# Kernel optimization log

Hardware: AMD Instinct MI355X
Metric: run time of the kernel (lower is better)

The kernel has to match this reference:

```python
import jax, jax.numpy as jnp
import numpy as np

B, S, D, H = 64, 128, 1024, 8
DK = D // H  # 128 == S, required by the module's (attn@V)@V quirk
DFF = 2048
EPS = 1e-12


def layernorm(x, w, b):
    u = x.mean(-1, keepdims=True)
    s = ((x - u) ** 2).mean(-1, keepdims=True)
    return w * (x - u) / jnp.sqrt(s + EPS) + b


def setup_inputs() -> dict:
    key = jax.random.key(0)
    ks = jax.random.split(key, 10)
    w = lambda k, shape: jax.random.normal(k, shape, jnp.float32) * 0.02
    return {
        "x": jax.random.normal(ks[0], (B, S, D), jnp.float32),
        "mask": jnp.ones((1, 1, S, S), jnp.int32),
        "Wq": w(ks[1], (D, D)), "bq": jnp.zeros((D,), jnp.float32),
        "Wk": w(ks[2], (D, D)), "bk": jnp.zeros((D,), jnp.float32),
        "Wv": w(ks[3], (D, D)), "bv": jnp.zeros((D,), jnp.float32),
        "Wo": w(ks[4], (D, D)), "bo": jnp.zeros((D,), jnp.float32),
        "ln1_w": jnp.ones((D,), jnp.float32), "ln1_b": jnp.zeros((D,), jnp.float32),
        "W1": w(ks[5], (DFF, D)), "b1": jnp.zeros((DFF,), jnp.float32),
        "W2": w(ks[6], (4 * D, DFF)), "b2": jnp.zeros((4 * D,), jnp.float32),
        "W3": w(ks[7], (D, 4 * D)), "b3": jnp.zeros((D,), jnp.float32),
        "ln2_w": jnp.ones((D,), jnp.float32), "ln2_b": jnp.zeros((D,), jnp.float32),
    }


def reference(x, mask, Wq, bq, Wk, bk, Wv, bv, Wo, bo, ln1_w, ln1_b,
              W1, b1, W2, b2, W3, b3, ln2_w, ln2_b):
    # QKV projections -> [B, H, S, DK]
    Q = (x @ Wq.T + bq).reshape(B, S, H, DK).transpose(0, 2, 1, 3)
    K = (x @ Wk.T + bk).reshape(B, S, H, DK).transpose(0, 2, 1, 3)
    V = (x @ Wv.T + bv).reshape(B, S, H, DK).transpose(0, 2, 1, 3)

    scores = jnp.einsum('bhqd,bhkd->bhqk', Q, K) / jnp.sqrt(jnp.float32(DK))
    scores = jnp.where(mask == 0, jnp.float32(-1e9), scores)
    attn = jax.nn.softmax(scores, axis=-1)  # dropout = identity (eval)
    av = jnp.matmul(attn, V)                 # [B,H,S,DK]
    # Faithful quirk in the source: multiply by V a second time (DK == S).
    ctx = jnp.matmul(av, V)                  # [B,H,S,DK]
    ctx = ctx.transpose(0, 2, 1, 3).reshape(B, S, D)
    attn_out = ctx @ Wo.T + bo

    h = layernorm(x + attn_out, ln1_w, ln1_b)

    f = jax.nn.relu(h @ W1.T + b1)           # [B,S,DFF]
    f = jax.nn.relu(f @ W2.T + b2)           # [B,S,4D]
    f = f @ W3.T + b3                        # [B,S,D]

    return layernorm(h + f, ln2_w, ln2_b)
```

## Files before the change

### kernel.cpp

```cpp
#include <hip/hip_runtime.h>
#include <hip/hip_bf16.h>

using bf16 = __hip_bfloat16;
typedef __attribute__((ext_vector_type(4))) float f32x4;
typedef __attribute__((ext_vector_type(8))) short bf16x8;

__device__ __forceinline__ unsigned short bfbits(float f) {
    bf16 h = __float2bfloat16(f);
    return __builtin_bit_cast(unsigned short, h);
}

__device__ __forceinline__ void g2l16(const void* g, void* l) {
    __builtin_amdgcn_global_load_lds(
        (const __attribute__((address_space(1))) unsigned int*)g,
        (__attribute__((address_space(3))) unsigned int*)l, 16, 0, 0);
}

__global__ void castk(const float* __restrict__ in, bf16* __restrict__ out, int n4) {
    int stride = gridDim.x * blockDim.x;
    for (int i = blockIdx.x * blockDim.x + threadIdx.x; i < n4; i += stride) {
        float4 v = reinterpret_cast<const float4*>(in)[i];
        ushort4 o;
        o.x = bfbits(v.x); o.y = bfbits(v.y); o.z = bfbits(v.z); o.w = bfbits(v.w);
        reinterpret_cast<ushort4*>(out)[i] = o;
    }
}

template<int EPI, int SPLITK>
__global__ __launch_bounds__(512, 2)
void gemm256(const bf16* __restrict__ A, const bf16* __restrict__ Bm,
             int N, int ldk, int kloop,
             const float* __restrict__ bias0, const float* __restrict__ bias1,
             const float* __restrict__ bias2,
             void* __restrict__ outp,
             bf16* __restrict__ q_o, bf16* __restrict__ k_o, bf16* __restrict__ v_o) {
    __shared__ __align__(16) char lds[65536];
    const int tid = threadIdx.x;
    const int lane = tid & 63, wave = tid >> 6;
    const int rlo = lane & 15, g = lane >> 4;
    const int wr = wave >> 2, wc = wave & 3;
    const int nbn = N >> 8;
    const int nwg = gridDim.x;
    int wg = (int)blockIdx.x;
    wg = (wg & 7) * (nwg >> 3) + (wg >> 3);
    int slice = 0;
    if constexpr (SPLITK) {
        int half = nwg >> 1;
        slice = (wg >= half) ? 1 : 0;
        wg -= slice * half;
    }
    const int bm = wg / nbn, bn = wg % nbn;
    const size_t ldb = (size_t)ldk * 2;
    const char* abase = (const char*)A + ((size_t)bm << 8) * ldb + (size_t)slice * kloop * 2;
    const char* bbase = (const char*)Bm + ((size_t)bn << 8) * ldb + (size_t)slice * kloop * 2;

    const int P = tid * 16;
    const int R = P >> 7;
    const int qs = (P & 127) ^ ((R & 7) << 4);
    const size_t goff0 = (size_t)(R * 2 + (qs >> 6)) * ldb + (qs & 63);
    const size_t ghalf = (size_t)128 * ldb;

    const int o_in = (((rlo & 1) << 6) | (g << 4)) ^ (((rlo >> 1) & 7) << 4);
    const int aoff = wr * 8192 + (rlo >> 1) * 128 + o_in;
    const int boff = 16384 + (wc >> 1) * 8192 + (wc & 1) * 4096 + (rlo >> 1) * 128 + o_in;

    const f32x4 fz = {0.f, 0.f, 0.f, 0.f};
    f32x4 acc[8][4];
#pragma unroll
    for (int i = 0; i < 8; ++i)
#pragma unroll
        for (int j = 0; j < 4; ++j) acc[i][j] = fz;

    auto stA = [&](int buf, int h, int kt) {
        g2l16(abase + goff0 + (size_t)h * ghalf + (size_t)kt * 64,
              lds + buf * 32768 + h * 8192 + P);
    };
    auto stB = [&](int buf, int h, int kt) {
        g2l16(bbase + goff0 + (size_t)h * ghalf + (size_t)kt * 64,
              lds + buf * 32768 + 16384 + h * 8192 + P);
    };

    stA(0, 0, 0); stA(0, 1, 0); stB(0, 0, 0); stB(0, 1, 0);
    asm volatile("s_waitcnt vmcnt(0)" ::: "memory");
    __builtin_amdgcn_s_barrier();
    __builtin_amdgcn_sched_barrier(0);

    const int NT = kloop >> 5;
    for (int kt = 0; kt < NT; ++kt) {
        const char* lb = lds + (kt & 1) * 32768;
        const int nbuf = (kt & 1) ^ 1;
        const bool pre = (kt + 1) < NT;

        bf16x8 bfr[4], afr[8];
#pragma unroll
        for (int nf = 0; nf < 4; ++nf)
            bfr[nf] = *reinterpret_cast<const bf16x8*>(lb + nf * 1024 + boff);
#pragma unroll
        for (int i = 0; i < 8; ++i)
            afr[i] = *reinterpret_cast<const bf16x8*>(lb + i * 1024 + aoff);
        if (pre) { stA(nbuf, 0, kt + 1); stA(nbuf, 1, kt + 1);
                   stB(nbuf, 0, kt + 1); stB(nbuf, 1, kt + 1); }
        __builtin_amdgcn_s_setprio(1);
#pragma unroll
        for (int i = 0; i < 4; ++i)
#pragma unroll
            for (int nf = 0; nf < 4; ++nf)
                acc[i][nf] = __builtin_amdgcn_mfma_f32_16x16x32_bf16(afr[i], bfr[nf], acc[i][nf], 0, 0, 0);
#pragma unroll
        for (int i = 0; i < 4; ++i)
#pragma unroll
            for (int nf = 0; nf < 4; ++nf)
                acc[4 + i][nf] = __builtin_amdgcn_mfma_f32_16x16x32_bf16(afr[4 + i], bfr[nf], acc[4 + i][nf], 0, 0, 0);
        __builtin_amdgcn_s_setprio(0);

        if (pre) {
            asm volatile("s_waitcnt vmcnt(0)" ::: "memory");
            __builtin_amdgcn_s_barrier();
            __builtin_amdgcn_sched_barrier(0);
        }
    }

    const int gm0 = (bm << 8) + wr * 128;
    const int gn0 = (bn << 8) + wc * 64;
#pragma unroll
    for (int mf = 0; mf < 8; ++mf) {
#pragma unroll
        for (int nf = 0; nf < 4; ++nf) {
            const int gnc = gn0 + nf * 16 + rlo;
#pragma unroll
            for (int r = 0; r < 4; ++r) {
                const int gmr = gm0 + mf * 16 + g * 4 + r;
                float val = acc[mf][nf][r];
                if constexpr (EPI == 0) {
                    int t = gnc >> 10;
                    const float* bp = (t == 0) ? bias0 : ((t == 1) ? bias1 : bias2);
                    val += bp[gnc & 1023];
                    bf16* dst = (t == 0) ? q_o : ((t == 1) ? k_o : v_o);
                    int hh = (gnc >> 7) & 7, d = gnc & 127;
                    int bb = gmr >> 7, s = gmr & 127;
                    dst[(((size_t)bb * 8 + hh) * 128 + s) * 128 + d] = __float2bfloat16(val);
                } else if constexpr (EPI == 1) {
                    val = fmaxf(val + bias0[gnc], 0.f);
                    ((bf16*)outp)[(size_t)gmr * N + gnc] = __float2bfloat16(val);
                } else {
                    float* pp = (float*)outp + (size_t)slice * 8388608;
                    pp[(size_t)gmr * N + gnc] = val;
                }
            }
        }
    }
}

template<int EPI>
__global__ __launch_bounds__(256, 2)
void gemm_bt(const bf16* __restrict__ A, const bf16* __restrict__ Bm,
             int M, int N, int K,
             const float* __restrict__ bias0, const float* __restrict__ resid,
             void* __restrict__ outp) {
    (void)M;
    __shared__ __align__(16) char As[8192];
    __shared__ __align__(16) char Bs[8192];
    int tid = threadIdx.x, wave = tid >> 6, lane = tid & 63;
    int nbn = N >> 7;
    int bm = blockIdx.x / nbn, bn = blockIdx.x % nbn;
    int wm = (wave >> 1) << 6, wn = (wave & 1) << 6;
    int rlo = lane & 15, g = lane >> 4;

    const char* abase = (const char*)(A + (size_t)(bm << 7) * K);
    const char* bbase = (const char*)(Bm + (size_t)(bn << 7) * K);

    const f32x4 fzero = {0.f, 0.f, 0.f, 0.f};
    f32x4 acc[4][4];
#pragma unroll
    for (int i = 0; i < 4; ++i)
#pragma unroll
        for (int j = 0; j < 4; ++j) acc[i][j] = fzero;

    int L0 = wave * 2048 + lane * 16;
    size_t ldbyte = (size_t)K * 2;

    for (int k0 = 0; k0 < K; k0 += 32) {
#pragma unroll
        for (int j = 0; j < 2; ++j) {
            int L = L0 + j * 1024;
            int row = L >> 6;
            int cb = (L & 63) ^ (((row >> 1) & 3) << 4);
            g2l16(abase + (size_t)row * ldbyte + (size_t)k0 * 2 + cb, As + wave * 2048 + j * 1024);
            g2l16(bbase + (size_t)row * ldbyte + (size_t)k0 * 2 + cb, Bs + wave * 2048 + j * 1024);
        }
        __syncthreads();
        bf16x8 af[4], bf8[4];
#pragma unroll
        for (int i = 0; i < 4; ++i) {
            int ra = wm + i * 16 + rlo;
            af[i] = *reinterpret_cast<const bf16x8*>(As + ra * 64 + ((g * 16) ^ (((ra >> 1) & 3) << 4)));
            int rb = wn + i * 16 + rlo;
            bf8[i] = *reinterpret_cast<const bf16x8*>(Bs + rb * 64 + ((g * 16) ^ (((rb >> 1) & 3) << 4)));
        }
#pragma unroll
        for (int mi = 0; mi < 4; ++mi)
#pragma unroll
            for (int ni = 0; ni < 4; ++ni)
                acc[mi][ni] = __builtin_amdgcn_mfma_f32_16x16x32_bf16(af[mi], bf8[ni], acc[mi][ni], 0, 0, 0);
        __syncthreads();
    }

    int gm0 = (bm << 7) + wm, gn0 = (bn << 7) + wn;
#pragma unroll
    for (int mi = 0; mi < 4; ++mi) {
#pragma unroll
        for (int ni = 0; ni < 4; ++ni) {
            int gnc = gn0 + ni * 16 + rlo;
#pragma unroll
            for (int r = 0; r < 4; ++r) {
                int gmr = gm0 + mi * 16 + g * 4 + r;
                float val = acc[mi][ni][r];
                val += bias0[gnc] + resid[(size_t)gmr * N + gnc];
                ((float*)outp)[(size_t)gmr * N + gnc] = val;
            }
        }
    }
}

__global__ __launch_bounds__(256)
void transpose_v(const bf16* __restrict__ V, bf16* __restrict__ VT) {
    __shared__ unsigned short t[128 * 132];
    int bh = blockIdx.x, tid = threadIdx.x;
    const unsigned short* src = (const unsigned short*)(V + (size_t)bh * 16384);
#pragma unroll
    for (int i = 0; i < 8; ++i) {
        int idx = tid + i * 256;
        int srow = idx >> 4;
        int c8 = (idx & 15) * 8;
        ushort4 a = reinterpret_cast<const ushort4*>(src + srow * 128 + c8)[0];
        ushort4 b = reinterpret_cast<const ushort4*>(src + srow * 128 + c8 + 4)[0];
        reinterpret_cast<ushort4*>(t + srow * 132 + c8)[0] = a;
        reinterpret_cast<ushort4*>(t + srow * 132 + c8 + 4)[0] = b;
    }
    __syncthreads();
    unsigned short* dst = (unsigned short*)(VT + (size_t)bh * 16384);
#pragma unroll
    for (int i = 0; i < 8; ++i) {
        int idx = tid + i * 256;
        int drow = idx >> 4;
        int s8 = (idx & 15) * 8;
        ushort4 a, b;
        a.x = t[(s8 + 0) * 132 + drow]; a.y = t[(s8 + 1) * 132 + drow];
        a.z = t[(s8 + 2) * 132 + drow]; a.w = t[(s8 + 3) * 132 + drow];
        b.x = t[(s8 + 4) * 132 + drow]; b.y = t[(s8 + 5) * 132 + drow];
        b.z = t[(s8 + 6) * 132 + drow]; b.w = t[(s8 + 7) * 132 + drow];
        reinterpret_cast<ushort4*>(dst + drow * 128 + s8)[0] = a;
        reinterpret_cast<ushort4*>(dst + drow * 128 + s8 + 4)[0] = b;
    }
}

__global__ __launch_bounds__(256, 2)
void attn_scores(const bf16* __restrict__ Q, const bf16* __restrict__ K, bf16* __restrict__ P) {
    __shared__ __align__(16) char Qs[32768];
    __shared__ __align__(16) char Ks[32768];
    int bh = blockIdx.x;
    int tid = threadIdx.x, wave = tid >> 6, lane = tid & 63;
    const char* qsrc = (const char*)(Q + (size_t)bh * 16384);
    const char* ksrc = (const char*)(K + (size_t)bh * 16384);
#pragma unroll
    for (int j = 0; j < 8; ++j) {
        int L = wave * 8192 + j * 1024 + lane * 16;
        int row = L >> 8;
        int cb = (L & 255) ^ ((row & 7) << 4);
        g2l16(qsrc + row * 256 + cb, Qs + wave * 8192 + j * 1024);
        g2l16(ksrc + row * 256 + cb, Ks + wave * 8192 + j * 1024);
    }
    __syncthreads();
    int rlo = lane & 15, g = lane >> 4;
    const f32x4 fzero = {0.f, 0.f, 0.f, 0.f};
    f32x4 acc[2][8];
#pragma unroll
    for (int mi = 0; mi < 2; ++mi)
#pragma unroll
        for (int ni = 0; ni < 8; ++ni) acc[mi][ni] = fzero;
#pragma unroll
    for (int kk = 0; kk < 4; ++kk) {
        bf16x8 aq[2], bk8[8];
#pragma unroll
        for (int mi = 0; mi < 2; ++mi) {
            int row = wave * 32 + mi * 16 + rlo;
            aq[mi] = *reinterpret_cast<const bf16x8*>(Qs + row * 256 + ((kk * 64 + g * 16) ^ ((row & 7) << 4)));
        }
#pragma unroll
        for (int ni = 0; ni < 8; ++ni) {
            int row = ni * 16 + rlo;
            bk8[ni] = *reinterpret_cast<const bf16x8*>(Ks + row * 256 + ((kk * 64 + g * 16) ^ ((row & 7) << 4)));
        }
#pragma unroll
        for (int mi = 0; mi < 2; ++mi)
#pragma unroll
            for (int ni = 0; ni < 8; ++ni)
                acc[mi][ni] = __builtin_amdgcn_mfma_f32_16x16x32_bf16(aq[mi], bk8[ni], acc[mi][ni], 0, 0, 0);
    }
    const float scale = 0.088388347648318447f;
    unsigned short* pdst = (unsigned short*)(P + (size_t)bh * 16384);
#pragma unroll
    for (int mi = 0; mi < 2; ++mi) {
#pragma unroll
        for (int r = 0; r < 4; ++r) {
            float m = -3e38f;
#pragma unroll
            for (int ni = 0; ni < 8; ++ni) m = fmaxf(m, acc[mi][ni][r]);
#pragma unroll
            for (int o = 1; o < 16; o <<= 1) m = fmaxf(m, __shfl_xor(m, o));
            m *= scale;
            float e[8];
            float sum = 0.f;
#pragma unroll
            for (int ni = 0; ni < 8; ++ni) { e[ni] = __expf(acc[mi][ni][r] * scale - m); sum += e[ni]; }
#pragma unroll
            for (int o = 1; o < 16; o <<= 1) sum += __shfl_xor(sum, o);
            float inv = 1.f / sum;
            int qrow = wave * 32 + mi * 16 + g * 4 + r;
#pragma unroll
            for (int ni = 0; ni < 8; ++ni)
                pdst[qrow * 128 + ni * 16 + rlo] = bfbits(e[ni] * inv);
        }
    }
}

__global__ __launch_bounds__(256, 2)
void attn_ctx(const bf16* __restrict__ P, const bf16* __restrict__ VT, bf16* __restrict__ CTX) {
    __shared__ __align__(16) char Vs[32768];
    __shared__ __align__(16) char Ts[32768];
    int bh = blockIdx.x, b = bh >> 3, h = bh & 7;
    int tid = threadIdx.x, wave = tid >> 6, lane = tid & 63;
    const char* vsrc = (const char*)(VT + (size_t)bh * 16384);
#pragma unroll
    for (int j = 0; j < 8; ++j) {
        int L = wave * 8192 + j * 1024 + lane * 16;
        int row = L >> 8;
        int cb = (L & 255) ^ ((row & 7) << 4);
        g2l16(vsrc + row * 256 + cb, Vs + wave * 8192 + j * 1024);
    }
    __syncthreads();
    int rlo = lane & 15, g = lane >> 4;
    const char* psrc = (const char*)(P + (size_t)bh * 16384);
    const f32x4 fzero = {0.f, 0.f, 0.f, 0.f};
    f32x4 accT[2][8];
#pragma unroll
    for (int mi = 0; mi < 2; ++mi)
#pragma unroll
        for (int ni = 0; ni < 8; ++ni) accT[mi][ni] = fzero;
#pragma unroll
    for (int kk = 0; kk < 4; ++kk) {
        bf16x8 ap[2], bv8[8];
#pragma unroll
        for (int mi = 0; mi < 2; ++mi) {
            int row = wave * 32 + mi * 16 + rlo;
            ap[mi] = *reinterpret_cast<const bf16x8*>(psrc + (size_t)row * 256 + kk * 64 + g * 16);
        }
#pragma unroll
        for (int ni = 0; ni < 8; ++ni) {
            int row = ni * 16 + rlo;
            bv8[ni] = *reinterpret_cast<const bf16x8*>(Vs + row * 256 + ((kk * 64 + g * 16) ^ ((row & 7) << 4)));
        }
#pragma unroll
        for (int mi = 0; mi < 2; ++mi)
#pragma unroll
            for (int ni = 0; ni < 8; ++ni)
                accT[mi][ni] = __builtin_amdgcn_mfma_f32_16x16x32_bf16(ap[mi], bv8[ni], accT[mi][ni], 0, 0, 0);
    }
#pragma unroll
    for (int mi = 0; mi < 2; ++mi)
#pragma unroll
        for (int ni = 0; ni < 8; ++ni)
#pragma unroll
            for (int r = 0; r < 4; ++r) {
                int trow = wave * 32 + mi * 16 + g * 4 + r;
                int cbyte = ((ni * 16 + rlo) * 2) ^ ((trow & 7) << 4);
                *(unsigned short*)(Ts + trow * 256 + cbyte) = bfbits(accT[mi][ni][r]);
            }
    __syncthreads();
    f32x4 accC[2][8];
#pragma unroll
    for (int mi = 0; mi < 2; ++mi)
#pragma unroll
        for (int ni = 0; ni < 8; ++ni) accC[mi][ni] = fzero;
#pragma unroll
    for (int kk = 0; kk < 4; ++kk) {
        bf16x8 at[2], bv8[8];
#pragma unroll
        for (int mi = 0; mi < 2; ++mi) {
            int row = wave * 32 + mi * 16 + rlo;
            at[mi] = *reinterpret_cast<const bf16x8*>(Ts + row * 256 + ((kk * 64 + g * 16) ^ ((row & 7) << 4)));
        }
#pragma unroll
        for (int ni = 0; ni < 8; ++ni) {
            int row = ni * 16 + rlo;
            bv8[ni] = *reinterpret_cast<const bf16x8*>(Vs + row * 256 + ((kk * 64 + g * 16) ^ ((row & 7) << 4)));
        }
#pragma unroll
        for (int mi = 0; mi < 2; ++mi)
#pragma unroll
            for (int ni = 0; ni < 8; ++ni)
                accC[mi][ni] = __builtin_amdgcn_mfma_f32_16x16x32_bf16(at[mi], bv8[ni], accC[mi][ni], 0, 0, 0);
    }
    unsigned short* cdst = (unsigned short*)CTX;
#pragma unroll
    for (int mi = 0; mi < 2; ++mi)
#pragma unroll
        for (int ni = 0; ni < 8; ++ni)
#pragma unroll
            for (int r = 0; r < 4; ++r) {
                int q = wave * 32 + mi * 16 + g * 4 + r;
                int gm = b * 128 + q;
                int col = h * 128 + ni * 16 + rlo;
                cdst[(size_t)gm * 1024 + col] = bfbits(accC[mi][ni][r]);
            }
}

template<int MODE>
__global__ __launch_bounds__(256)
void ln_k(const float* __restrict__ Y, const float* __restrict__ w, const float* __restrict__ b,
          float* __restrict__ Hf, bf16* __restrict__ Hb) {
    int row = blockIdx.x, tid = threadIdx.x;
    float4 v = reinterpret_cast<const float4*>(Y + (size_t)row * 1024)[tid];
    float s = v.x + v.y + v.z + v.w;
    float q = v.x * v.x + v.y * v.y + v.z * v.z + v.w * v.w;
#pragma unroll
    for (int o = 1; o < 64; o <<= 1) { s += __shfl_xor(s, o); q += __shfl_xor(q, o); }
    __shared__ float ss[4], sq[4];
    if ((tid & 63) == 0) { ss[tid >> 6] = s; sq[tid >> 6] = q; }
    __syncthreads();
    s = ss[0] + ss[1] + ss[2] + ss[3];
    q = sq[0] + sq[1] + sq[2] + sq[3];
    float u = s * (1.f / 1024.f);
    float var = fmaxf(q * (1.f / 1024.f) - u * u, 0.f);
    float rstd = rsqrtf(var + 1e-12f);
    float4 wv = reinterpret_cast<const float4*>(w)[tid];
    float4 bv = reinterpret_cast<const float4*>(b)[tid];
    float o0 = wv.x * (v.x - u) * rstd + bv.x;
    float o1 = wv.y * (v.y - u) * rstd + bv.y;
    float o2 = wv.z * (v.z - u) * rstd + bv.z;
    float o3 = wv.w * (v.w - u) * rstd + bv.w;
    reinterpret_cast<float4*>(Hf + (size_t)row * 1024)[tid] = make_float4(o0, o1, o2, o3);
    if constexpr (MODE == 0) {
        ushort4 ob;
        ob.x = bfbits(o0); ob.y = bfbits(o1); ob.z = bfbits(o2); ob.w = bfbits(o3);
        reinterpret_cast<ushort4*>(Hb)[row * 256 + tid] = ob;
    }
}

__global__ __launch_bounds__(256)
void ln2k(const float* __restrict__ PA, const float* __restrict__ PB,
          const float* __restrict__ b3, const float* __restrict__ resid,
          const float* __restrict__ w, const float* __restrict__ b,
          float* __restrict__ out) {
    int row = blockIdx.x, tid = threadIdx.x;
    size_t off = (size_t)row * 256 + tid;
    float4 pa = reinterpret_cast<const float4*>(PA)[off];
    float4 pb = reinterpret_cast<const float4*>(PB)[off];
    float4 bi = reinterpret_cast<const float4*>(b3)[tid];
    float4 rs = reinterpret_cast<const float4*>(resid)[off];
    float4 v = make_float4(pa.x + pb.x + bi.x + rs.x, pa.y + pb.y + bi.y + rs.y,
                           pa.z + pb.z + bi.z + rs.z, pa.w + pb.w + bi.w + rs.w);
    float s = v.x + v.y + v.z + v.w;
    float q = v.x * v.x + v.y * v.y + v.z * v.z + v.w * v.w;
#pragma unroll
    for (int o = 1; o < 64; o <<= 1) { s += __shfl_xor(s, o); q += __shfl_xor(q, o); }
    __shared__ float ss[4], sq[4];
    if ((tid & 63) == 0) { ss[tid >> 6] = s; sq[tid >> 6] = q; }
    __syncthreads();
    s = ss[0] + ss[1] + ss[2] + ss[3];
    q = sq[0] + sq[1] + sq[2] + sq[3];
    float u = s * (1.f / 1024.f);
    float var = fmaxf(q * (1.f / 1024.f) - u * u, 0.f);
    float rstd = rsqrtf(var + 1e-12f);
    float4 wv = reinterpret_cast<const float4*>(w)[tid];
    float4 bv = reinterpret_cast<const float4*>(b)[tid];
    float4 o4;
    o4.x = wv.x * (v.x - u) * rstd + bv.x;
    o4.y = wv.y * (v.y - u) * rstd + bv.y;
    o4.z = wv.z * (v.z - u) * rstd + bv.z;
    o4.w = wv.w * (v.w - u) * rstd + bv.w;
    reinterpret_cast<float4*>(out)[off] = o4;
}

extern "C" void kernel_launch(void* const* d_in, const int* in_sizes, int n_in,
                              void* d_out, int out_size, void* d_ws, size_t ws_size,
                              hipStream_t stream) {
    (void)in_sizes; (void)n_in; (void)out_size; (void)ws_size;
    const float* x    = (const float*)d_in[0];
    const float* Wq   = (const float*)d_in[2];
    const float* bq   = (const float*)d_in[3];
    const float* Wk   = (const float*)d_in[4];
    const float* bk   = (const float*)d_in[5];
    const float* Wv   = (const float*)d_in[6];
    const float* bv   = (const float*)d_in[7];
    const float* Wo   = (const float*)d_in[8];
    const float* bo   = (const float*)d_in[9];
    const float* ln1w = (const float*)d_in[10];
    const float* ln1b = (const float*)d_in[11];
    const float* W1   = (const float*)d_in[12];
    const float* b1   = (const float*)d_in[13];
    const float* W2   = (const float*)d_in[14];
    const float* b2   = (const float*)d_in[15];
    const float* W3   = (const float*)d_in[16];
    const float* b3   = (const float*)d_in[17];
    const float* ln2w = (const float*)d_in[18];
    const float* ln2b = (const float*)d_in[19];

    char* ws = (char*)d_ws;
    bf16*  XB    = (bf16*)(ws + 0);
    bf16*  WQKVB = (bf16*)(ws + 16777216);
    bf16*  WOB   = (bf16*)(ws + 23068672);
    bf16*  W1B   = (bf16*)(ws + 25165824);
    bf16*  W2B   = (bf16*)(ws + 29360128);
    bf16*  W3B   = (bf16*)(ws + 46137344);
    bf16*  Qb    = (bf16*)(ws + 54525952);
    bf16*  Kb    = (bf16*)(ws + 71303168);
    bf16*  Vb    = (bf16*)(ws + 88080384);
    bf16*  VTb   = (bf16*)(ws + 104857600);
    bf16*  Pb    = (bf16*)(ws + 121634816);
    bf16*  CTX   = (bf16*)(ws + 138412032);
    float* Y2    = (float*)(ws + 155189248);
    float* H32   = (float*)(ws + 188743680);
    bf16*  HB    = (bf16*)(ws + 222298112);
    bf16*  F1    = (bf16*)(ws + 155189248);
    bf16*  F2    = (bf16*)(ws + 54525952);
    float* PW3   = (float*)(ws + 121634816);

    auto cast = [&](const float* s, bf16* dd, int n4) {
        int nb = (n4 + 255) / 256; if (nb > 2048) nb = 2048;
        castk<<<nb, 256, 0, stream>>>(s, dd, n4);
    };
    cast(x,  XB,             2097152);
    cast(Wq, WQKVB,           262144);
    cast(Wk, WQKVB + 1048576, 262144);
    cast(Wv, WQKVB + 2097152, 262144);
    cast(Wo, WOB,             262144);
    cast(W1, W1B,             524288);
    cast(W2, W2B,            2097152);
    cast(W3, W3B,            1048576);

    gemm256<0, 0><<<384, 512, 0, stream>>>(XB, WQKVB, 3072, 1024, 1024,
                                           bq, bk, bv, nullptr, Qb, Kb, Vb);
    transpose_v<<<512, 256, 0, stream>>>(Vb, VTb);
    attn_scores<<<512, 256, 0, stream>>>(Qb, Kb, Pb);
    attn_ctx<<<512, 256, 0, stream>>>(Pb, VTb, CTX);
    gemm_bt<2><<<512, 256, 0, stream>>>(CTX, WOB, 8192, 1024, 1024, bo, x, (void*)Y2);
    ln_k<0><<<8192, 256, 0, stream>>>(Y2, ln1w, ln1b, H32, HB);
    gemm256<1, 0><<<256, 512, 0, stream>>>(HB, W1B, 2048, 1024, 1024,
                                           b1, nullptr, nullptr, (void*)F1, nullptr, nullptr, nullptr);
    gemm256<1, 0><<<512, 512, 0, stream>>>(F1, W2B, 4096, 2048, 2048,
                                           b2, nullptr, nullptr, (void*)F2, nullptr, nullptr, nullptr);
    gemm256<2, 1><<<256, 512, 0, stream>>>(F2, W3B, 1024, 4096, 2048,
                                           nullptr, nullptr, nullptr, (void*)PW3, nullptr, nullptr, nullptr);
    ln2k<<<8192, 256, 0, stream>>>(PW3, PW3 + 8388608, b3, H32, ln2w, ln2b, (float*)d_out);
}
```

Measured before the change: 459.2 us.

## Deepen GEMM K-tile to 64 with 4-phase interleaved LDS staging pipeline

The 256x256 bf16 GEMM kernel now uses a 64-wide K tile with 128KB of LDS double buffering. Each iteration is split into four MFMA phases interleaved with partial LDS fragment loads and staggered global-to-LDS prefetches. A is prefetched two tiles ahead and B one tile ahead. The aim is to halve loop iterations and hide global and LDS latency behind MFMA work. In exchange it adds many more barriers, and 128KB of LDS likely drops occupancy from 2 workgroups per CU to 1.

```diff
diff --git a/kernel.cpp b/kernel.cpp
--- a/kernel.cpp
+++ b/kernel.cpp
@@ -34,7 +34,7 @@
              const float* __restrict__ bias2,
              void* __restrict__ outp,
              bf16* __restrict__ q_o, bf16* __restrict__ k_o, bf16* __restrict__ v_o) {
-    __shared__ __align__(16) char lds[65536];
+    __shared__ __align__(16) char lds[131072];
     const int tid = threadIdx.x;
     const int lane = tid & 63, wave = tid >> 6;
     const int rlo = lane & 15, g = lane >> 4;
@@ -54,15 +54,38 @@
     const char* abase = (const char*)A + ((size_t)bm << 8) * ldb + (size_t)slice * kloop * 2;
     const char* bbase = (const char*)Bm + ((size_t)bn << 8) * ldb + (size_t)slice * kloop * 2;
 
-    const int P = tid * 16;
-    const int R = P >> 7;
-    const int qs = (P & 127) ^ ((R & 7) << 4);
-    const size_t goff0 = (size_t)(R * 2 + (qs >> 6)) * ldb + (qs & 63);
-    const size_t ghalf = (size_t)128 * ldb;
-
-    const int o_in = (((rlo & 1) << 6) | (g << 4)) ^ (((rlo >> 1) & 7) << 4);
-    const int aoff = wr * 8192 + (rlo >> 1) * 128 + o_in;
-    const int boff = 16384 + (wc >> 1) * 8192 + (wc & 1) * 4096 + (rlo >> 1) * 128 + o_in;
+    auto stage = [&](int bufbyte, int region, int h, const char* gbase, int kt) {
+#pragma unroll
+        for (int j = 0; j < 2; ++j) {
+            int P = tid * 16 + j * 8192;
+            int row = P >> 7;
+            int col = (P & 127) ^ ((row & 7) << 4);
+            g2l16(gbase + (size_t)(h * 128 + row) * ldb + (size_t)kt * 128 + col,
+                  lds + bufbyte + region * 32768 + h * 16384 + P);
+        }
+    };
+
+    const int sw = (rlo & 7) << 4;
+    const int c0 = (g * 16) ^ sw;
+    const int c1 = (64 | (g * 16)) ^ sw;
+
+    auto ldA = [&](const char* lb, int q, bf16x8* ar) {
+#pragma unroll
+        for (int i = 0; i < 4; ++i) {
+            const char* rp = lb + wr * 16384 + ((q * 4 + i) * 16 + rlo) * 128;
+            ar[i * 2 + 0] = *reinterpret_cast<const bf16x8*>(rp + c0);
+            ar[i * 2 + 1] = *reinterpret_cast<const bf16x8*>(rp + c1);
+        }
+    };
+    auto ldB = [&](const char* lb, int p, bf16x8* br) {
+#pragma unroll
+        for (int j = 0; j < 2; ++j) {
+            const char* rp = lb + 32768 + (wc >> 1) * 16384 +
+                             ((wc & 1) * 64 + (p * 2 + j) * 16 + rlo) * 128;
+            br[j * 2 + 0] = *reinterpret_cast<const bf16x8*>(rp + c0);
+            br[j * 2 + 1] = *reinterpret_cast<const bf16x8*>(rp + c1);
+        }
+    };
 
     const f32x4 fz = {0.f, 0.f, 0.f, 0.f};
     f32x4 acc[8][4];
@@ -71,50 +94,86 @@
 #pragma unroll
         for (int j = 0; j < 4; ++j) acc[i][j] = fz;
 
-    auto stA = [&](int buf, int h, int kt) {
-        g2l16(abase + goff0 + (size_t)h * ghalf + (size_t)kt * 64,
-              lds + buf * 32768 + h * 8192 + P);
-    };
-    auto stB = [&](int buf, int h, int kt) {
-        g2l16(bbase + goff0 + (size_t)h * ghalf + (size_t)kt * 64,
-              lds + buf * 32768 + 16384 + h * 8192 + P);
-    };
-
-    stA(0, 0, 0); stA(0, 1, 0); stB(0, 0, 0); stB(0, 1, 0);
-    asm volatile("s_waitcnt vmcnt(0)" ::: "memory");
+    const int NT = kloop >> 6;
+
+    stage(0, 0, 0, abase, 0); stage(0, 0, 1, abase, 0);
+    stage(0, 1, 0, bbase, 0); stage(0, 1, 1, bbase, 0);
+    stage(65536, 0, 0, abase, 1); stage(65536, 0, 1, abase, 1);
+    asm volatile("s_waitcnt vmcnt(4)" ::: "memory");
     __builtin_amdgcn_s_barrier();
     __builtin_amdgcn_sched_barrier(0);
 
-    const int NT = kloop >> 5;
-    for (int kt = 0; kt < NT; ++kt) {
-        const char* lb = lds + (kt & 1) * 32768;
-        const int nbuf = (kt & 1) ^ 1;
-        const bool pre = (kt + 1) < NT;
-
-        bf16x8 bfr[4], afr[8];
-#pragma unroll
-        for (int nf = 0; nf < 4; ++nf)
-            bfr[nf] = *reinterpret_cast<const bf16x8*>(lb + nf * 1024 + boff);
-#pragma unroll
-        for (int i = 0; i < 8; ++i)
-            afr[i] = *reinterpret_cast<const bf16x8*>(lb + i * 1024 + aoff);
-        if (pre) { stA(nbuf, 0, kt + 1); stA(nbuf, 1, kt + 1);
-                   stB(nbuf, 0, kt + 1); stB(nbuf, 1, kt + 1); }
+    for (int t = 0; t < NT; ++t) {
+        const int cbb = (t & 1) * 65536;
+        const int obb = cbb ^ 65536;
+        const char* lb = lds + cbb;
+        bf16x8 a0[8], a1[8], b[4];
+
+        ldA(lb, 0, a0); ldB(lb, 0, b);
+        if (t + 1 < NT) stage(obb, 1, 0, bbase, t + 1);
+        __builtin_amdgcn_s_barrier();
+        asm volatile("s_waitcnt lgkmcnt(0)" ::: "memory");
+        __builtin_amdgcn_sched_barrier(0);
         __builtin_amdgcn_s_setprio(1);
 #pragma unroll
         for (int i = 0; i < 4; ++i)
 #pragma unroll
-            for (int nf = 0; nf < 4; ++nf)
-                acc[i][nf] = __builtin_amdgcn_mfma_f32_16x16x32_bf16(afr[i], bfr[nf], acc[i][nf], 0, 0, 0);
+            for (int j = 0; j < 2; ++j)
+#pragma unroll
+                for (int ks = 0; ks < 2; ++ks)
+                    acc[i][j] = __builtin_amdgcn_mfma_f32_16x16x32_bf16(a0[i*2+ks], b[j*2+ks], acc[i][j], 0, 0, 0);
+        __builtin_amdgcn_s_setprio(0);
+        __builtin_amdgcn_s_barrier();
+
+        ldA(lb, 1, a1);
+        if (t + 1 < NT) stage(obb, 1, 1, bbase, t + 1);
+        __builtin_amdgcn_s_barrier();
+        asm volatile("s_waitcnt lgkmcnt(0)" ::: "memory");
+        __builtin_amdgcn_sched_barrier(0);
+        __builtin_amdgcn_s_setprio(1);
 #pragma unroll
         for (int i = 0; i < 4; ++i)
 #pragma unroll
-            for (int nf = 0; nf < 4; ++nf)
-                acc[4 + i][nf] = __builtin_amdgcn_mfma_f32_16x16x32_bf16(afr[4 + i], bfr[nf], acc[4 + i][nf], 0, 0, 0);
+            for (int j = 0; j < 2; ++j)
+#pragma unroll
+                for (int ks = 0; ks < 2; ++ks)
+                    acc[4+i][j] = __builtin_amdgcn_mfma_f32_16x16x32_bf16(a1[i*2+ks], b[j*2+ks], acc[4+i][j], 0, 0, 0);
         __builtin_amdgcn_s_setprio(0);
-
-        if (pre) {
-            asm volatile("s_waitcnt vmcnt(0)" ::: "memory");
+        __builtin_amdgcn_s_barrier();
+
+        ldB(lb, 1, b);
+        if (t + 2 < NT) stage(cbb, 0, 0, abase, t + 2);
+        __builtin_amdgcn_s_barrier();
+        asm volatile("s_waitcnt lgkmcnt(0)" ::: "memory");
+        __builtin_amdgcn_sched_barrier(0);
+        __builtin_amdgcn_s_setprio(1);
+#pragma unroll
+        for (int i = 0; i < 4; ++i)
+#pragma unroll
+            for (int j = 0; j < 2; ++j)
+#pragma unroll
+                for (int ks = 0; ks < 2; ++ks)
+                    acc[4+i][2+j] = __builtin_amdgcn_mfma_f32_16x16x32_bf16(a1[i*2+ks], b[j*2+ks], acc[4+i][2+j], 0, 0, 0);
+        __builtin_amdgcn_s_setprio(0);
+        __builtin_amdgcn_s_barrier();
+
+        if (t + 2 < NT) stage(cbb, 0, 1, abase, t + 2);
+        if (t + 1 < NT) {
+            if (t + 2 < NT) { asm volatile("s_waitcnt vmcnt(4)" ::: "memory"); }
+            else            { asm volatile("s_waitcnt vmcnt(0)" ::: "memory"); }
+        }
+        __builtin_amdgcn_s_barrier();
+        __builtin_amdgcn_sched_barrier(0);
+        __builtin_amdgcn_s_setprio(1);
+#pragma unroll
+        for (int i = 0; i < 4; ++i)
+#pragma unroll
+            for (int j = 0; j < 2; ++j)
+#pragma unroll
+                for (int ks = 0; ks < 2; ++ks)
+                    acc[i][2+j] = __builtin_amdgcn_mfma_f32_16x16x32_bf16(a0[i*2+ks], b[j*2+ks], acc[i][2+j], 0, 0, 0);
+        __builtin_amdgcn_s_setprio(0);
+        if (t + 1 < NT) {
             __builtin_amdgcn_s_barrier();
             __builtin_amdgcn_sched_barrier(0);
         }
```

After: 434.2 us. 5.4% less time.

## Triple-buffer LDS in GEMM and prefetch next-tile fragments into registers

Applied to the files above, without the earlier changes.

Moves the bf16 GEMM main loop from a double-buffered LDS scheme to three 32KB LDS stages. Global-to-LDS copies are issued two tiles ahead, and the A/B fragments for the next k-tile are read from LDS between the two MFMA halves, so LDS reads overlap with matrix math. The aim is to hide global-load and LDS-read latency behind compute. The cost is LDS per block growing from 64KB to 96KB, which together with launch_bounds(512,2) likely leaves room for only one resident block per CU. The loop also still waits on vmcnt(0) every iteration, which limits how far ahead the loads can actually run.

```diff
diff --git a/kernel.cpp b/kernel.cpp
--- a/kernel.cpp
+++ b/kernel.cpp
@@ -34,7 +34,7 @@
              const float* __restrict__ bias2,
              void* __restrict__ outp,
              bf16* __restrict__ q_o, bf16* __restrict__ k_o, bf16* __restrict__ v_o) {
-    __shared__ __align__(16) char lds[65536];
+    __shared__ __align__(16) char lds[98304];
     const int tid = threadIdx.x;
     const int lane = tid & 63, wave = tid >> 6;
     const int rlo = lane & 15, g = lane >> 4;
@@ -71,52 +71,65 @@
 #pragma unroll
         for (int j = 0; j < 4; ++j) acc[i][j] = fz;
 
-    auto stA = [&](int buf, int h, int kt) {
-        g2l16(abase + goff0 + (size_t)h * ghalf + (size_t)kt * 64,
-              lds + buf * 32768 + h * 8192 + P);
+    auto stage_tile = [&](int bufb, int kt) {
+        g2l16(abase + goff0 + (size_t)kt * 64,          lds + bufb + P);
+        g2l16(abase + goff0 + ghalf + (size_t)kt * 64,  lds + bufb + 8192 + P);
+        g2l16(bbase + goff0 + (size_t)kt * 64,          lds + bufb + 16384 + P);
+        g2l16(bbase + goff0 + ghalf + (size_t)kt * 64,  lds + bufb + 24576 + P);
     };
-    auto stB = [&](int buf, int h, int kt) {
-        g2l16(bbase + goff0 + (size_t)h * ghalf + (size_t)kt * 64,
-              lds + buf * 32768 + 16384 + h * 8192 + P);
-    };
-
-    stA(0, 0, 0); stA(0, 1, 0); stB(0, 0, 0); stB(0, 1, 0);
-    asm volatile("s_waitcnt vmcnt(0)" ::: "memory");
+
+    const int NT = kloop >> 5;
+
+    bf16x8 a[8], b[4];
+
+    stage_tile(0, 0);
+    stage_tile(32768, 1);
+    asm volatile("s_waitcnt vmcnt(4)" ::: "memory");
     __builtin_amdgcn_s_barrier();
     __builtin_amdgcn_sched_barrier(0);
-
-    const int NT = kloop >> 5;
-    for (int kt = 0; kt < NT; ++kt) {
-        const char* lb = lds + (kt & 1) * 32768;
-        const int nbuf = (kt & 1) ^ 1;
-        const bool pre = (kt + 1) < NT;
-
-        bf16x8 bfr[4], afr[8];
-#pragma unroll
-        for (int nf = 0; nf < 4; ++nf)
-            bfr[nf] = *reinterpret_cast<const bf16x8*>(lb + nf * 1024 + boff);
-#pragma unroll
-        for (int i = 0; i < 8; ++i)
-            afr[i] = *reinterpret_cast<const bf16x8*>(lb + i * 1024 + aoff);
-        if (pre) { stA(nbuf, 0, kt + 1); stA(nbuf, 1, kt + 1);
-                   stB(nbuf, 0, kt + 1); stB(nbuf, 1, kt + 1); }
-        __builtin_amdgcn_s_setprio(1);
-#pragma unroll
-        for (int i = 0; i < 4; ++i)
-#pragma unroll
-            for (int nf = 0; nf < 4; ++nf)
-                acc[i][nf] = __builtin_amdgcn_mfma_f32_16x16x32_bf16(afr[i], bfr[nf], acc[i][nf], 0, 0, 0);
-#pragma unroll
-        for (int i = 0; i < 4; ++i)
-#pragma unroll
-            for (int nf = 0; nf < 4; ++nf)
-                acc[4 + i][nf] = __builtin_amdgcn_mfma_f32_16x16x32_bf16(afr[4 + i], bfr[nf], acc[4 + i][nf], 0, 0, 0);
-        __builtin_amdgcn_s_setprio(0);
-
-        if (pre) {
+#pragma unroll
+    for (int i = 0; i < 8; ++i)
+        a[i] = *reinterpret_cast<const bf16x8*>(lds + i * 1024 + aoff);
+#pragma unroll
+    for (int j = 0; j < 4; ++j)
+        b[j] = *reinterpret_cast<const bf16x8*>(lds + j * 1024 + boff);
+
+    for (int t = 0; t < NT; ++t) {
+        const bool hn = (t + 1) < NT;
+        if (hn) {
             asm volatile("s_waitcnt vmcnt(0)" ::: "memory");
             __builtin_amdgcn_s_barrier();
             __builtin_amdgcn_sched_barrier(0);
+        }
+        if (t + 2 < NT) stage_tile(((t + 2) % 3) * 32768, t + 2);
+        const char* lbn = lds + ((t + 1) % 3) * 32768;
+
+        __builtin_amdgcn_s_setprio(1);
+#pragma unroll
+        for (int mf = 0; mf < 4; ++mf)
+#pragma unroll
+            for (int nf = 0; nf < 4; ++nf)
+                acc[mf][nf] = __builtin_amdgcn_mfma_f32_16x16x32_bf16(a[mf], b[nf], acc[mf][nf], 0, 0, 0);
+        __builtin_amdgcn_s_setprio(0);
+        if (hn) {
+#pragma unroll
+            for (int i = 0; i < 4; ++i)
+                a[i] = *reinterpret_cast<const bf16x8*>(lbn + i * 1024 + aoff);
+        }
+        __builtin_amdgcn_s_setprio(1);
+#pragma unroll
+        for (int mf = 4; mf < 8; ++mf)
+#pragma unroll
+            for (int nf = 0; nf < 4; ++nf)
+                acc[mf][nf] = __builtin_amdgcn_mfma_f32_16x16x32_bf16(a[mf], b[nf], acc[mf][nf], 0, 0, 0);
+        __builtin_amdgcn_s_setprio(0);
+        if (hn) {
+#pragma unroll
+            for (int i = 4; i < 8; ++i)
+                a[i] = *reinterpret_cast<const bf16x8*>(lbn + i * 1024 + aoff);
+#pragma unroll
+            for (int j = 0; j < 4; ++j)
+                b[j] = *reinterpret_cast<const bf16x8*>(lbn + j * 1024 + boff);
         }
     }
 
```

New measurement: 451.7 us. No clear change (-1.6%).
